# Kernel tuning notes

Hardware: AMD Instinct MI355X
Metric: run time of the kernel (lower is better)

Reference implementation:

```python
import jax, jax.numpy as jnp
import numpy as np

EPS = 1e-08
ITERATIONS = 3


def squash(s):
    # s: [..., d]
    s2 = jnp.sum(s * s, axis=-1, keepdims=True)
    return s2 / (1.0 + s2) * (s / jnp.sqrt(s2 + EPS))


def setup_inputs() -> dict:
    key = jax.random.key(0)
    k1, k2 = jax.random.split(key)
    B, IN_CAPS, OUT_CAPS, IN_D, OUT_D = 256, 1152, 10, 8, 16
    u = jax.random.normal(k1, (B, IN_CAPS, IN_D), dtype=jnp.float32)
    weight = jax.random.normal(k2, (IN_CAPS, OUT_CAPS, IN_D, OUT_D), dtype=jnp.float32)
    return {"u": u, "weight": weight}


def reference(u, weight):
    # u: [B, in_caps, in_d]; weight: [in_caps, out_caps, in_d, out_d]
    u_hat = jnp.einsum('ijnm,bin->bijm', weight, u)  # [B, in_caps, out_caps, out_d]
    B, in_caps, out_caps, _ = u_hat.shape
    b = jnp.zeros((B, in_caps, out_caps), dtype=u.dtype)
    v = None
    for _ in range(ITERATIONS):
        c = jax.nn.softmax(b, axis=1)  # softmax over in_caps (dim=1, faithful to source)
        s = jnp.einsum('bij,bijm->bjm', c, u_hat)  # [B, out_caps, out_d]
        v = squash(s)
        a = jnp.einsum('bjm,bijm->bij', v, u_hat)
        b = b + a
    return v
```

## Files before the change

### kernel.cpp

```cpp
#include <hip/hip_runtime.h>
#include <hip/hip_bf16.h>
#include <math.h>


#define IC 1152
#define OC 10
#define NB 256

__device__ __forceinline__ float bf_lo(unsigned w) { return __uint_as_float(w << 16); }
__device__ __forceinline__ float bf_hi(unsigned w) { return __uint_as_float(w & 0xFFFF0000u); }
__device__ __forceinline__ unsigned pack2(float a, float b) {
    __hip_bfloat162 h = __float22bfloat162_rn(make_float2(a, b));
    return *(unsigned*)&h;
}
__device__ __forceinline__ unsigned short pack1(float a) {
    __hip_bfloat16 h = __float2bfloat16(a);
    return *(unsigned short*)&h;
}

__global__ __launch_bounds__(512, 4)
void caps_route_kernel(const float* __restrict__ u,
                       const float* __restrict__ W,
                       float* __restrict__ out) {
    extern __shared__ unsigned smem_u[];
    unsigned* uh = smem_u;
    unsigned short* ce = (unsigned short*)(uh + 2 * IC * 8);
    float* spart = (float*)(ce + 2 * IC);

    const int t    = threadIdx.x;
    const int bx   = blockIdx.x;
    const int lane = t & 63;
    const int wid  = t >> 6;

    int x = bx & 7, sg = bx >> 3;
    int j, p;
    if (sg < 128) { j = x; p = sg; }
    else { int s2 = sg - 128; j = 8 + (x >> 2); p = ((x & 3) << 5) + s2; }
    const int bb = p * 2;

    {
        const int q  = t & 3;
        const int i0 = t >> 2;
        const int pb = (((q >> 1) ^ ((i0 >> 2) & 1)) << 2) + ((q & 1) << 1);
        const float* u0p = u + (size_t)bb * (IC * 8);
#pragma unroll 3
        for (int k = 0; k < 9; ++k) {
            const int i = i0 + 128 * k;
            const float4* wrow = (const float4*)(W + ((size_t)(i * OC + j) << 7)) + q;
            const float4 ua0 = *(const float4*)(u0p + i * 8);
            const float4 ua1 = *(const float4*)(u0p + i * 8 + 4);
            const float4 ub0 = *(const float4*)(u0p + IC * 8 + i * 8);
            const float4 ub1 = *(const float4*)(u0p + IC * 8 + i * 8 + 4);
            float4 s0 = {0.f,0.f,0.f,0.f}, s1 = {0.f,0.f,0.f,0.f};
            float4 w4;
#define ST(ux, uy, n)                                                     \
            w4 = wrow[(n) * 4];                                           \
            s0.x += (ux)*w4.x; s0.y += (ux)*w4.y;                         \
            s0.z += (ux)*w4.z; s0.w += (ux)*w4.w;                         \
            s1.x += (uy)*w4.x; s1.y += (uy)*w4.y;                         \
            s1.z += (uy)*w4.z; s1.w += (uy)*w4.w;
            ST(ua0.x, ub0.x, 0) ST(ua0.y, ub0.y, 1) ST(ua0.z, ub0.z, 2) ST(ua0.w, ub0.w, 3)
            ST(ua1.x, ub1.x, 4) ST(ua1.y, ub1.y, 5) ST(ua1.z, ub1.z, 6) ST(ua1.w, ub1.w, 7)
#undef ST
            const int dst = (i << 3) + pb;
            *(uint2*)&uh[dst]          = make_uint2(pack2(s0.x, s0.y), pack2(s0.z, s0.w));
            *(uint2*)&uh[IC * 8 + dst] = make_uint2(pack2(s1.x, s1.y), pack2(s1.z, s1.w));
        }
    }

    __syncthreads();

    if (wid >= 4) {
        __syncthreads();
        __syncthreads();
        __syncthreads();
        return;
    }

    const int bt = wid & 1;
    const int hf = (wid >> 1) & 1;
    const unsigned* uhT = uh + bt * (IC * 8);
    unsigned short* ceT = ce + bt * IC;
    const int rowbase = hf * 576;

    const int mq = lane & 3;
    const int h  = lane >> 2;
    const int pbS = (((mq >> 1) ^ ((h >> 2) & 1)) << 2) + ((mq & 1) << 1);
    const bool eB = ((lane >> 2) & 1) != 0;

    float L[9];
#pragma unroll
    for (int k = 0; k < 9; ++k) L[k] = 0.f;

    for (int r = 0; r < 3; ++r) {
        float se = 0.f;
        if (r > 0) {
#pragma unroll
            for (int k = 0; k < 9; ++k) {
                const float ev = __expf(L[k]);
                ceT[rowbase + lane + 64 * k] = pack1(ev);
                se += ev;
            }
#pragma unroll
            for (int o = 32; o >= 1; o >>= 1) se += __shfl_xor(se, o, 64);
        }

        float4 acc = {0.f, 0.f, 0.f, 0.f};
        if (r == 0) {
#pragma unroll 6
            for (int k = 0; k < 36; ++k) {
                const int i = rowbase + 16 * k + h;
                const uint2 d = *(const uint2*)&uhT[(i << 3) + pbS];
                acc.x += bf_lo(d.x); acc.y += bf_hi(d.x);
                acc.z += bf_lo(d.y); acc.w += bf_hi(d.y);
            }
        } else {
#pragma unroll 6
            for (int k = 0; k < 36; ++k) {
                const int i = rowbase + 16 * k + h;
                const uint2 d = *(const uint2*)&uhT[(i << 3) + pbS];
                const float c = __uint_as_float(((unsigned)ceT[i]) << 16);
                acc.x += c * bf_lo(d.x); acc.y += c * bf_hi(d.x);
                acc.z += c * bf_lo(d.y); acc.w += c * bf_hi(d.y);
            }
        }
#pragma unroll
        for (int o = 4; o <= 32; o <<= 1) {
            acc.x += __shfl_xor(acc.x, o, 64);
            acc.y += __shfl_xor(acc.y, o, 64);
            acc.z += __shfl_xor(acc.z, o, 64);
            acc.w += __shfl_xor(acc.w, o, 64);
        }

        float* sp = spart + (r & 1) * 80 + bt * 40 + hf * 20;
        if (lane < 4) *(float4*)&sp[lane << 2] = acc;
        if (r > 0 && lane == 4) sp[16] = se;
        __syncthreads();
        const float* so = spart + (r & 1) * 80 + bt * 40 + (1 - hf) * 20;
        const float4 oq = *(const float4*)&so[mq << 2];
        const float inv = (r == 0) ? (1.0f / (float)IC) : 1.0f / (se + so[16]);
        const float4 s4 = make_float4((acc.x + oq.x) * inv, (acc.y + oq.y) * inv,
                                      (acc.z + oq.z) * inv, (acc.w + oq.w) * inv);

        float p2 = s4.x*s4.x + s4.y*s4.y + s4.z*s4.z + s4.w*s4.w;
        p2 += __shfl_xor(p2, 1, 64);
        p2 += __shfl_xor(p2, 2, 64);
        const float sc = p2 / ((1.0f + p2) * sqrtf(p2 + 1e-8f));
        const float4 vq = make_float4(s4.x * sc, s4.y * sc, s4.z * sc, s4.w * sc);

        if (r == 2) {
            if (hf == 0 && lane < 4)
                *(float4*)&out[((size_t)(bb + bt) * OC + j) * 16 + (lane << 2)] = vq;
        } else {
            const float4 q0 = make_float4(__shfl(vq.x, 0, 4), __shfl(vq.y, 0, 4),
                                          __shfl(vq.z, 0, 4), __shfl(vq.w, 0, 4));
            const float4 q1 = make_float4(__shfl(vq.x, 1, 4), __shfl(vq.y, 1, 4),
                                          __shfl(vq.z, 1, 4), __shfl(vq.w, 1, 4));
            const float4 q2 = make_float4(__shfl(vq.x, 2, 4), __shfl(vq.y, 2, 4),
                                          __shfl(vq.z, 2, 4), __shfl(vq.w, 2, 4));
            const float4 q3 = make_float4(__shfl(vq.x, 3, 4), __shfl(vq.y, 3, 4),
                                          __shfl(vq.z, 3, 4), __shfl(vq.w, 3, 4));
            const float4 Qa0 = eB ? q2 : q0, Qa1 = eB ? q3 : q1;
            const float4 Qb0 = eB ? q0 : q2, Qb1 = eB ? q1 : q3;
#pragma unroll 3
            for (int k = 0; k < 9; ++k) {
                const int i = rowbase + lane + 64 * k;
                const uint4 da = *(const uint4*)&uhT[i << 3];
                const uint4 db = *(const uint4*)&uhT[(i << 3) + 4];
                L[k] += bf_lo(da.x)*Qa0.x + bf_hi(da.x)*Qa0.y
                      + bf_lo(da.y)*Qa0.z + bf_hi(da.y)*Qa0.w
                      + bf_lo(da.z)*Qa1.x + bf_hi(da.z)*Qa1.y
                      + bf_lo(da.w)*Qa1.z + bf_hi(da.w)*Qa1.w
                      + bf_lo(db.x)*Qb0.x + bf_hi(db.x)*Qb0.y
                      + bf_lo(db.y)*Qb0.z + bf_hi(db.y)*Qb0.w
                      + bf_lo(db.z)*Qb1.x + bf_hi(db.z)*Qb1.y
                      + bf_lo(db.w)*Qb1.z + bf_hi(db.w)*Qb1.w;
            }
        }
    }
}

extern "C" void kernel_launch(void* const* d_in, const int* in_sizes, int n_in,
                              void* d_out, int out_size, void* d_ws, size_t ws_size,
                              hipStream_t stream) {
    const float* u = (const float*)d_in[0];
    const float* W = (const float*)d_in[1];
    float* out = (float*)d_out;

    const size_t shmem = (size_t)(2 * IC * 8) * 4 + (size_t)(2 * IC) * 2 + 160 * 4;
    hipFuncSetAttribute((const void*)caps_route_kernel,
                        hipFuncAttributeMaxDynamicSharedMemorySize, (int)shmem);

    caps_route_kernel<<<(NB / 2) * OC, 512, shmem, stream>>>(u, W, out);
}
```

Baseline: 121.3 us.

## Persistent blocks with warp-specialized double-buffered u_hat staging overlapping routing

Replaces the 1280-block launch with 256 persistent blocks, each processing 5 (batch-pair, out-cap) items. Two warps act as producers, computing the next item's u_hat into a second shared-memory buffer while six consumer warps run the three routing iterations on the current one. The routing work is now split across three warps per batch, and the exp/softmax write is fused into the logit update. Shared memory use doubles, which cuts occupancy to about 2 blocks per CU, and the two producer warps may become the bottleneck.

```diff
diff --git a/kernel.cpp b/kernel.cpp
--- a/kernel.cpp
+++ b/kernel.cpp
@@ -6,6 +6,9 @@
 #define IC 1152
 #define OC 10
 #define NB 256
+#define TILE_DW (IC * 8)
+#define NBLK 256
+#define IPB 5
 
 __device__ __forceinline__ float bf_lo(unsigned w) { return __uint_as_float(w << 16); }
 __device__ __forceinline__ float bf_hi(unsigned w) { return __uint_as_float(w & 0xFFFF0000u); }
@@ -18,165 +21,223 @@
     return *(unsigned short*)&h;
 }
 
-__global__ __launch_bounds__(512, 4)
+__device__ __forceinline__ void item_map(int it, int& j, int& bb) {
+    const int x = it & 7, sg = it >> 3;
+    int p;
+    if (sg < 128) { j = x; p = sg; }
+    else { const int s2 = sg - 128; j = 8 + (x >> 2); p = ((x & 3) << 5) + s2; }
+    bb = p * 2;
+}
+
+__device__ __forceinline__ void stage_row(unsigned* __restrict__ uhd,
+                                          const float* __restrict__ uB,
+                                          const float* __restrict__ W,
+                                          int j, int i, int mq, int pb) {
+    const float4* wrow = (const float4*)(W + ((size_t)(i * OC + j) << 7)) + mq;
+    const float* ur = uB + i * 8;
+    const float4 ua0 = *(const float4*)(ur);
+    const float4 ua1 = *(const float4*)(ur + 4);
+    const float4 ub0 = *(const float4*)(ur + IC * 8);
+    const float4 ub1 = *(const float4*)(ur + IC * 8 + 4);
+    float4 s0 = {0.f,0.f,0.f,0.f}, s1 = {0.f,0.f,0.f,0.f};
+    float4 w4;
+#define ST(ux, uy, n)                                                     \
+    w4 = wrow[(n) * 4];                                                   \
+    s0.x += (ux)*w4.x; s0.y += (ux)*w4.y; s0.z += (ux)*w4.z; s0.w += (ux)*w4.w; \
+    s1.x += (uy)*w4.x; s1.y += (uy)*w4.y; s1.z += (uy)*w4.z; s1.w += (uy)*w4.w;
+    ST(ua0.x, ub0.x, 0) ST(ua0.y, ub0.y, 1) ST(ua0.z, ub0.z, 2) ST(ua0.w, ub0.w, 3)
+    ST(ua1.x, ub1.x, 4) ST(ua1.y, ub1.y, 5) ST(ua1.z, ub1.z, 6) ST(ua1.w, ub1.w, 7)
+#undef ST
+    const int dst = (i << 3) + pb;
+    *(uint2*)&uhd[dst]           = make_uint2(pack2(s0.x, s0.y), pack2(s0.z, s0.w));
+    *(uint2*)&uhd[TILE_DW + dst] = make_uint2(pack2(s1.x, s1.y), pack2(s1.z, s1.w));
+}
+
+__global__ __launch_bounds__(512, 2)
 void caps_route_kernel(const float* __restrict__ u,
                        const float* __restrict__ W,
                        float* __restrict__ out) {
     extern __shared__ unsigned smem_u[];
-    unsigned* uh = smem_u;
-    unsigned short* ce = (unsigned short*)(uh + 2 * IC * 8);
+    unsigned* uh0 = smem_u;
+    unsigned* uh1 = smem_u + 2 * TILE_DW;
+    unsigned short* ce = (unsigned short*)(smem_u + 4 * TILE_DW);
     float* spart = (float*)(ce + 2 * IC);
 
     const int t    = threadIdx.x;
-    const int bx   = blockIdx.x;
     const int lane = t & 63;
     const int wid  = t >> 6;
-
-    int x = bx & 7, sg = bx >> 3;
-    int j, p;
-    if (sg < 128) { j = x; p = sg; }
-    else { int s2 = sg - 128; j = 8 + (x >> 2); p = ((x & 3) << 5) + s2; }
-    const int bb = p * 2;
+    const int blk  = blockIdx.x;
+
+    int j_cur, bb_cur;
+    item_map(blk, j_cur, bb_cur);
 
     {
-        const int q  = t & 3;
-        const int i0 = t >> 2;
-        const int pb = (((q >> 1) ^ ((i0 >> 2) & 1)) << 2) + ((q & 1) << 1);
-        const float* u0p = u + (size_t)bb * (IC * 8);
-#pragma unroll 3
-        for (int k = 0; k < 9; ++k) {
-            const int i = i0 + 128 * k;
-            const float4* wrow = (const float4*)(W + ((size_t)(i * OC + j) << 7)) + q;
-            const float4 ua0 = *(const float4*)(u0p + i * 8);
-            const float4 ua1 = *(const float4*)(u0p + i * 8 + 4);
-            const float4 ub0 = *(const float4*)(u0p + IC * 8 + i * 8);
-            const float4 ub1 = *(const float4*)(u0p + IC * 8 + i * 8 + 4);
-            float4 s0 = {0.f,0.f,0.f,0.f}, s1 = {0.f,0.f,0.f,0.f};
-            float4 w4;
-#define ST(ux, uy, n)                                                     \
-            w4 = wrow[(n) * 4];                                           \
-            s0.x += (ux)*w4.x; s0.y += (ux)*w4.y;                         \
-            s0.z += (ux)*w4.z; s0.w += (ux)*w4.w;                         \
-            s1.x += (uy)*w4.x; s1.y += (uy)*w4.y;                         \
-            s1.z += (uy)*w4.z; s1.w += (uy)*w4.w;
-            ST(ua0.x, ub0.x, 0) ST(ua0.y, ub0.y, 1) ST(ua0.z, ub0.z, 2) ST(ua0.w, ub0.w, 3)
-            ST(ua1.x, ub1.x, 4) ST(ua1.y, ub1.y, 5) ST(ua1.z, ub1.z, 6) ST(ua1.w, ub1.w, 7)
-#undef ST
-            const int dst = (i << 3) + pb;
-            *(uint2*)&uh[dst]          = make_uint2(pack2(s0.x, s0.y), pack2(s0.z, s0.w));
-            *(uint2*)&uh[IC * 8 + dst] = make_uint2(pack2(s1.x, s1.y), pack2(s1.z, s1.w));
-        }
+        const int mq = t & 3, i0 = t >> 2;
+        const int pb = (((mq >> 1) ^ ((i0 >> 2) & 1)) << 2) + ((mq & 1) << 1);
+        const float* uB = u + (size_t)bb_cur * (IC * 8);
+#pragma unroll 3
+        for (int k = 0; k < 9; ++k)
+            stage_row(uh0, uB, W, j_cur, i0 + 128 * k, mq, pb);
     }
-
     __syncthreads();
 
-    if (wid >= 4) {
-        __syncthreads();
-        __syncthreads();
-        __syncthreads();
-        return;
-    }
-
-    const int bt = wid & 1;
-    const int hf = (wid >> 1) & 1;
-    const unsigned* uhT = uh + bt * (IC * 8);
-    unsigned short* ceT = ce + bt * IC;
-    const int rowbase = hf * 576;
-
-    const int mq = lane & 3;
-    const int h  = lane >> 2;
-    const int pbS = (((mq >> 1) ^ ((h >> 2) & 1)) << 2) + ((mq & 1) << 1);
+    const int bt = (wid >= 3) ? 1 : 0;
+    const int w3 = wid - bt * 3;
+    const int rowbase = w3 * 384;
+    const int mqc = lane & 3;
+    const int h   = lane >> 2;
+    const int pbS = (((mqc >> 1) ^ ((h >> 2) & 1)) << 2) + ((mqc & 1) << 1);
     const bool eB = ((lane >> 2) & 1) != 0;
-
-    float L[9];
-#pragma unroll
-    for (int k = 0; k < 9; ++k) L[k] = 0.f;
-
-    for (int r = 0; r < 3; ++r) {
-        float se = 0.f;
-        if (r > 0) {
-#pragma unroll
-            for (int k = 0; k < 9; ++k) {
-                const float ev = __expf(L[k]);
-                ceT[rowbase + lane + 64 * k] = pack1(ev);
-                se += ev;
-            }
-#pragma unroll
-            for (int o = 32; o >= 1; o >>= 1) se += __shfl_xor(se, o, 64);
-        }
-
-        float4 acc = {0.f, 0.f, 0.f, 0.f};
-        if (r == 0) {
+    const int pw  = wid - 6;
+    const int ibp = pw * 576 + (lane >> 2);
+    const int pbP = (((mqc >> 1) ^ ((lane >> 4) & 1)) << 2) + ((mqc & 1) << 1);
+
+    for (int e = 0; e < IPB; ++e) {
+        unsigned* uh_cur = (e & 1) ? uh1 : uh0;
+        unsigned* uh_nxt = (e & 1) ? uh0 : uh1;
+        const bool hasNext = (e + 1 < IPB);
+        int j_nxt = j_cur, bb_nxt = bb_cur;
+        if (hasNext) item_map(blk + NBLK * (e + 1), j_nxt, bb_nxt);
+        const float* uBn = u + (size_t)bb_nxt * (IC * 8);
+
+        const unsigned* uhT = uh_cur + bt * TILE_DW;
+        unsigned short* ceT = ce + bt * IC;
+        float* spB0 = spart + bt * 60;
+        float* spB1 = spart + 120 + bt * 60;
+
+        float4 acc = {0.f,0.f,0.f,0.f};
+        float  se  = 0.f;
+        float  L[6];
+        float4 vq  = {0.f,0.f,0.f,0.f};
+
+        auto spass_c = [&]() {
+            acc = make_float4(0.f, 0.f, 0.f, 0.f);
 #pragma unroll 6
-            for (int k = 0; k < 36; ++k) {
-                const int i = rowbase + 16 * k + h;
-                const uint2 d = *(const uint2*)&uhT[(i << 3) + pbS];
-                acc.x += bf_lo(d.x); acc.y += bf_hi(d.x);
-                acc.z += bf_lo(d.y); acc.w += bf_hi(d.y);
-            }
-        } else {
-#pragma unroll 6
-            for (int k = 0; k < 36; ++k) {
+            for (int k = 0; k < 24; ++k) {
                 const int i = rowbase + 16 * k + h;
                 const uint2 d = *(const uint2*)&uhT[(i << 3) + pbS];
                 const float c = __uint_as_float(((unsigned)ceT[i]) << 16);
                 acc.x += c * bf_lo(d.x); acc.y += c * bf_hi(d.x);
                 acc.z += c * bf_lo(d.y); acc.w += c * bf_hi(d.y);
             }
-        }
-#pragma unroll
-        for (int o = 4; o <= 32; o <<= 1) {
-            acc.x += __shfl_xor(acc.x, o, 64);
-            acc.y += __shfl_xor(acc.y, o, 64);
-            acc.z += __shfl_xor(acc.z, o, 64);
-            acc.w += __shfl_xor(acc.w, o, 64);
-        }
-
-        float* sp = spart + (r & 1) * 80 + bt * 40 + hf * 20;
-        if (lane < 4) *(float4*)&sp[lane << 2] = acc;
-        if (r > 0 && lane == 4) sp[16] = se;
-        __syncthreads();
-        const float* so = spart + (r & 1) * 80 + bt * 40 + (1 - hf) * 20;
-        const float4 oq = *(const float4*)&so[mq << 2];
-        const float inv = (r == 0) ? (1.0f / (float)IC) : 1.0f / (se + so[16]);
-        const float4 s4 = make_float4((acc.x + oq.x) * inv, (acc.y + oq.y) * inv,
-                                      (acc.z + oq.z) * inv, (acc.w + oq.w) * inv);
-
-        float p2 = s4.x*s4.x + s4.y*s4.y + s4.z*s4.z + s4.w*s4.w;
-        p2 += __shfl_xor(p2, 1, 64);
-        p2 += __shfl_xor(p2, 2, 64);
-        const float sc = p2 / ((1.0f + p2) * sqrtf(p2 + 1e-8f));
-        const float4 vq = make_float4(s4.x * sc, s4.y * sc, s4.z * sc, s4.w * sc);
-
-        if (r == 2) {
-            if (hf == 0 && lane < 4)
-                *(float4*)&out[((size_t)(bb + bt) * OC + j) * 16 + (lane << 2)] = vq;
-        } else {
-            const float4 q0 = make_float4(__shfl(vq.x, 0, 4), __shfl(vq.y, 0, 4),
-                                          __shfl(vq.z, 0, 4), __shfl(vq.w, 0, 4));
-            const float4 q1 = make_float4(__shfl(vq.x, 1, 4), __shfl(vq.y, 1, 4),
-                                          __shfl(vq.z, 1, 4), __shfl(vq.w, 1, 4));
-            const float4 q2 = make_float4(__shfl(vq.x, 2, 4), __shfl(vq.y, 2, 4),
-                                          __shfl(vq.z, 2, 4), __shfl(vq.w, 2, 4));
-            const float4 q3 = make_float4(__shfl(vq.x, 3, 4), __shfl(vq.y, 3, 4),
-                                          __shfl(vq.z, 3, 4), __shfl(vq.w, 3, 4));
+#pragma unroll
+            for (int o = 4; o <= 32; o <<= 1) {
+                acc.x += __shfl_xor(acc.x, o, 64); acc.y += __shfl_xor(acc.y, o, 64);
+                acc.z += __shfl_xor(acc.z, o, 64); acc.w += __shfl_xor(acc.w, o, 64);
+            }
+        };
+        auto combine = [&](const float* spB, int r) {
+            const int o1 = ((w3 + 1) % 3) * 20, o2 = ((w3 + 2) % 3) * 20;
+            const float4 q1 = *(const float4*)&spB[o1 + (mqc << 2)];
+            const float4 q2 = *(const float4*)&spB[o2 + (mqc << 2)];
+            const float inv = (r == 0) ? (1.0f / (float)IC)
+                                       : 1.0f / (se + spB[o1 + 16] + spB[o2 + 16]);
+            const float4 s4 = make_float4((acc.x + q1.x + q2.x) * inv,
+                                          (acc.y + q1.y + q2.y) * inv,
+                                          (acc.z + q1.z + q2.z) * inv,
+                                          (acc.w + q1.w + q2.w) * inv);
+            float p2 = s4.x*s4.x + s4.y*s4.y + s4.z*s4.z + s4.w*s4.w;
+            p2 += __shfl_xor(p2, 1, 64);
+            p2 += __shfl_xor(p2, 2, 64);
+            const float sc = p2 / ((1.0f + p2) * sqrtf(p2 + 1e-8f));
+            vq = make_float4(s4.x * sc, s4.y * sc, s4.z * sc, s4.w * sc);
+        };
+        auto bupd_exp = [&]() {
+            const float4 q0 = make_float4(__shfl(vq.x,0,4), __shfl(vq.y,0,4),
+                                          __shfl(vq.z,0,4), __shfl(vq.w,0,4));
+            const float4 q1 = make_float4(__shfl(vq.x,1,4), __shfl(vq.y,1,4),
+                                          __shfl(vq.z,1,4), __shfl(vq.w,1,4));
+            const float4 q2 = make_float4(__shfl(vq.x,2,4), __shfl(vq.y,2,4),
+                                          __shfl(vq.z,2,4), __shfl(vq.w,2,4));
+            const float4 q3 = make_float4(__shfl(vq.x,3,4), __shfl(vq.y,3,4),
+                                          __shfl(vq.z,3,4), __shfl(vq.w,3,4));
             const float4 Qa0 = eB ? q2 : q0, Qa1 = eB ? q3 : q1;
             const float4 Qb0 = eB ? q0 : q2, Qb1 = eB ? q1 : q3;
-#pragma unroll 3
-            for (int k = 0; k < 9; ++k) {
+            se = 0.f;
+#pragma unroll 3
+            for (int k = 0; k < 6; ++k) {
                 const int i = rowbase + lane + 64 * k;
                 const uint4 da = *(const uint4*)&uhT[i << 3];
                 const uint4 db = *(const uint4*)&uhT[(i << 3) + 4];
-                L[k] += bf_lo(da.x)*Qa0.x + bf_hi(da.x)*Qa0.y
-                      + bf_lo(da.y)*Qa0.z + bf_hi(da.y)*Qa0.w
-                      + bf_lo(da.z)*Qa1.x + bf_hi(da.z)*Qa1.y
-                      + bf_lo(da.w)*Qa1.z + bf_hi(da.w)*Qa1.w
-                      + bf_lo(db.x)*Qb0.x + bf_hi(db.x)*Qb0.y
-                      + bf_lo(db.y)*Qb0.z + bf_hi(db.y)*Qb0.w
-                      + bf_lo(db.z)*Qb1.x + bf_hi(db.z)*Qb1.y
-                      + bf_lo(db.w)*Qb1.z + bf_hi(db.w)*Qb1.w;
-            }
-        }
+                const float dot = bf_lo(da.x)*Qa0.x + bf_hi(da.x)*Qa0.y
+                                + bf_lo(da.y)*Qa0.z + bf_hi(da.y)*Qa0.w
+                                + bf_lo(da.z)*Qa1.x + bf_hi(da.z)*Qa1.y
+                                + bf_lo(da.w)*Qa1.z + bf_hi(da.w)*Qa1.w
+                                + bf_lo(db.x)*Qb0.x + bf_hi(db.x)*Qb0.y
+                                + bf_lo(db.y)*Qb0.z + bf_hi(db.y)*Qb0.w
+                                + bf_lo(db.z)*Qb1.x + bf_hi(db.z)*Qb1.y
+                                + bf_lo(db.w)*Qb1.z + bf_hi(db.w)*Qb1.w;
+                L[k] += dot;
+                const float ev = __expf(L[k]);
+                ceT[i] = pack1(ev);
+                se += ev;
+            }
+#pragma unroll
+            for (int o = 32; o >= 1; o >>= 1) se += __shfl_xor(se, o, 64);
+        };
+
+        if (wid < 6) {
+#pragma unroll
+            for (int k = 0; k < 6; ++k) L[k] = 0.f;
+            acc = make_float4(0.f, 0.f, 0.f, 0.f);
+#pragma unroll 6
+            for (int k = 0; k < 24; ++k) {
+                const int i = rowbase + 16 * k + h;
+                const uint2 d = *(const uint2*)&uhT[(i << 3) + pbS];
+                acc.x += bf_lo(d.x); acc.y += bf_hi(d.x);
+                acc.z += bf_lo(d.y); acc.w += bf_hi(d.y);
+            }
+#pragma unroll
+            for (int o = 4; o <= 32; o <<= 1) {
+                acc.x += __shfl_xor(acc.x, o, 64); acc.y += __shfl_xor(acc.y, o, 64);
+                acc.z += __shfl_xor(acc.z, o, 64); acc.w += __shfl_xor(acc.w, o, 64);
+            }
+            if (lane < 4) *(float4*)&spB0[w3 * 20 + (lane << 2)] = acc;
+        } else if (hasNext) {
+#pragma unroll 3
+            for (int kk = 0; kk < 9; ++kk)
+                stage_row(uh_nxt, uBn, W, j_nxt, ibp + 16 * kk, mqc, pbP);
+        }
+        __syncthreads();
+
+        if (wid < 6) {
+            combine(spB0, 0);
+            bupd_exp();
+            spass_c();
+            if (lane < 4) *(float4*)&spB1[w3 * 20 + (lane << 2)] = acc;
+            else if (lane == 4) spB1[w3 * 20 + 16] = se;
+        } else if (hasNext) {
+#pragma unroll 3
+            for (int kk = 9; kk < 18; ++kk)
+                stage_row(uh_nxt, uBn, W, j_nxt, ibp + 16 * kk, mqc, pbP);
+        }
+        __syncthreads();
+
+        if (wid < 6) {
+            combine(spB1, 1);
+            bupd_exp();
+            spass_c();
+            if (lane < 4) *(float4*)&spB0[w3 * 20 + (lane << 2)] = acc;
+            else if (lane == 4) spB0[w3 * 20 + 16] = se;
+        } else if (hasNext) {
+#pragma unroll 3
+            for (int kk = 18; kk < 27; ++kk)
+                stage_row(uh_nxt, uBn, W, j_nxt, ibp + 16 * kk, mqc, pbP);
+        }
+        __syncthreads();
+
+        if (wid < 6) {
+            combine(spB0, 2);
+            if (w3 == 0 && lane < 4)
+                *(float4*)&out[((size_t)(bb_cur + bt) * OC + j_cur) * 16 + (lane << 2)] = vq;
+        } else if (hasNext) {
+#pragma unroll 3
+            for (int kk = 27; kk < 36; ++kk)
+                stage_row(uh_nxt, uBn, W, j_nxt, ibp + 16 * kk, mqc, pbP);
+        }
+        __syncthreads();
+
+        j_cur = j_nxt; bb_cur = bb_nxt;
     }
 }
 
@@ -187,9 +248,11 @@
     const float* W = (const float*)d_in[1];
     float* out = (float*)d_out;
 
-    const size_t shmem = (size_t)(2 * IC * 8) * 4 + (size_t)(2 * IC) * 2 + 160 * 4;
+    const size_t shmem = (size_t)4 * TILE_DW * 4
+                       + (size_t)2 * IC * 2
+                       + 240 * 4;
     hipFuncSetAttribute((const void*)caps_route_kernel,
                         hipFuncAttributeMaxDynamicSharedMemorySize, (int)shmem);
 
-    caps_route_kernel<<<(NB / 2) * OC, 512, shmem, stream>>>(u, W, out);
-}
+    caps_route_kernel<<<NBLK, 512, shmem, stream>>>(u, W, out);
+}
```

Result: slower. 274.7 us (+126.4%).
